# Kernel optimization log

Hardware: AMD Instinct MI355X
Metric: run time of the kernel (lower is better)

The kernel has to match this reference:

```python
import jax, jax.numpy as jnp
import numpy as np

D_MODEL, D_STATE, D_CONV, EXPAND = 1024, 16, 4, 2
D_INNER = EXPAND * D_MODEL
DT_RANK = (D_MODEL + 15) // 16  # 64
B_SZ, SEQ = 2, 1024


def _mamba_dir(x, inW, convW, convB, xpW, dtW, dtB, Alog, Dp, outW):
    """Standard Mamba block forward. x: [B, L, d_model]."""
    Bsz, L, _ = x.shape
    d_inner, d_state = Alog.shape
    dt_rank = xpW.shape[0] - 2 * d_state
    xz = jnp.einsum('bld,ed->ble', x, inW)            # [B, L, 2*d_inner]
    xi, z = jnp.split(xz, 2, axis=-1)
    # depthwise causal conv along L
    xc = jnp.swapaxes(xi, 1, 2)                       # [B, d_inner, L]
    xc = jax.lax.conv_general_dilated(
        xc, convW, window_strides=(1,),
        padding=[(convW.shape[-1] - 1, 0)],
        feature_group_count=d_inner)
    xc = xc + convB[None, :, None]
    u = jax.nn.silu(jnp.swapaxes(xc, 1, 2))           # [B, L, d_inner]
    x_dbl = jnp.einsum('bld,ed->ble', u, xpW)         # [B, L, dt_rank+2N]
    dt, Bm, Cm = jnp.split(x_dbl, [dt_rank, dt_rank + d_state], axis=-1)
    delta = jax.nn.softplus(jnp.einsum('blr,dr->bld', dt, dtW) + dtB)  # [B,L,d_inner]
    A = -jnp.exp(Alog)                                # [d_inner, d_state]

    def step(h, ins):
        d_t, B_t, C_t, u_t = ins                      # [B,D],[B,N],[B,N],[B,D]
        dA = jnp.exp(d_t[:, :, None] * A)             # [B, D, N]
        h = h * dA + (d_t * u_t)[:, :, None] * B_t[:, None, :]
        y_t = jnp.einsum('bdn,bn->bd', h, C_t)
        return h, y_t

    h0 = jnp.zeros((Bsz, d_inner, d_state), x.dtype)
    xs = (jnp.swapaxes(delta, 0, 1), jnp.swapaxes(Bm, 0, 1),
          jnp.swapaxes(Cm, 0, 1), jnp.swapaxes(u, 0, 1))
    _, ys = jax.lax.scan(step, h0, xs)
    y = jnp.swapaxes(ys, 0, 1)                        # [B, L, d_inner]
    y = y + u * Dp
    y = y * jax.nn.silu(z)
    return jnp.einsum('bld,od->blo', y, outW)         # [B, L, d_model]


def _make_params(key, suffix):
    ks = jax.random.split(key, 10)
    s = 0.02
    p = {
        'inW' + suffix: jax.random.normal(ks[0], (2 * D_INNER, D_MODEL), jnp.float32) * s,
        'convW' + suffix: jax.random.normal(ks[1], (D_INNER, 1, D_CONV), jnp.float32) * s,
        'convB' + suffix: jnp.zeros((D_INNER,), jnp.float32),
        'xpW' + suffix: jax.random.normal(ks[2], (DT_RANK + 2 * D_STATE, D_INNER), jnp.float32) * s,
        'dtW' + suffix: jax.random.normal(ks[3], (D_INNER, DT_RANK), jnp.float32) * s,
        'dtB' + suffix: jax.random.normal(ks[4], (D_INNER,), jnp.float32) * 0.1 - 4.0,
        'Alog' + suffix: jnp.log(1.0 + jax.random.uniform(ks[5], (D_INNER, D_STATE), jnp.float32) * 15.0),
        'Dp' + suffix: jnp.ones((D_INNER,), jnp.float32),
        'outW' + suffix: jax.random.normal(ks[6], (D_MODEL, D_INNER), jnp.float32) * s,
    }
    return p


def setup_inputs() -> dict:
    key = jax.random.key(0)
    kx, kf, kb = jax.random.split(key, 3)
    inp = {'x': jax.random.normal(kx, (B_SZ, SEQ, D_MODEL), jnp.float32)}
    inp.update(_make_params(kf, '_f'))
    inp.update(_make_params(kb, '_b'))
    return inp


def reference(x, inW_f, convW_f, convB_f, xpW_f, dtW_f, dtB_f, Alog_f, Dp_f, outW_f,
              inW_b, convW_b, convB_b, xpW_b, dtW_b, dtB_b, Alog_b, Dp_b, outW_b):
    y_fwd = _mamba_dir(x, inW_f, convW_f, convB_f, xpW_f, dtW_f, dtB_f, Alog_f, Dp_f, outW_f)
    xb = jnp.flip(x, axis=1)
    y_bwd = jnp.flip(_mamba_dir(xb, inW_b, convW_b, convB_b, xpW_b, dtW_b, dtB_b, Alog_b, Dp_b, outW_b), axis=1)
    return 0.5 * (y_fwd + y_bwd)
```

## Files before the change

### kernel.cpp

```cpp
#include <hip/hip_runtime.h>
#include <math.h>

#define B_SZ 2
#define SEQ  1024
#define DM   1024
#define DI   2048
#define NST  16
#define RNK  64
#define XPD  96
#define M_TOT (B_SZ*SEQ)
#define NC   32
#define LC   (SEQ/NC)
#define NCH  65536

typedef unsigned short ushort_t;
typedef __attribute__((ext_vector_type(8))) short short8;
typedef __attribute__((ext_vector_type(4))) float f32x4;

#if __has_builtin(__builtin_amdgcn_exp2f)
#define EXP2F __builtin_amdgcn_exp2f
#else
#define EXP2F exp2f
#endif
#define LOG2E 1.44269504f

__device__ __forceinline__ ushort_t f2bf(float f) {
    unsigned u = __float_as_uint(f);
    u += 0x7fff + ((u >> 16) & 1);
    return (ushort_t)(u >> 16);
}
__device__ __forceinline__ float bf2f(ushort_t v) {
    return __uint_as_float(((unsigned)v) << 16);
}

__global__ __launch_bounds__(256)
void convert_all(const float* __restrict__ x,
                 const float* __restrict__ inWf, const float* __restrict__ inWb,
                 const float* __restrict__ outWf, const float* __restrict__ outWb,
                 const float* __restrict__ xpWf, const float* __restrict__ xpWb,
                 ushort_t* __restrict__ xbf, ushort_t* __restrict__ inWcat,
                 ushort_t* __restrict__ outWcat, ushort_t* __restrict__ xpWcat)
{
    int bid = blockIdx.x;
    const float* src; ushort_t* dst; int rel; int strided = 0;
    if (bid < 2048)       { rel = bid;         src = x;     dst = xbf; }
    else if (bid < 6144)  { rel = bid - 2048;  src = inWf;  dst = inWcat; }
    else if (bid < 10240) { rel = bid - 6144;  src = inWb;  dst = inWcat + (size_t)2 * DI * DM; }
    else if (bid < 12288) { rel = bid - 10240; src = outWf; dst = outWcat;      strided = 1; }
    else if (bid < 14336) { rel = bid - 12288; src = outWb; dst = outWcat + DI; strided = 1; }
    else if (bid < 14528) { rel = bid - 14336; src = xpWf;  dst = xpWcat; }
    else                  { rel = bid - 14528; src = xpWb;  dst = xpWcat + (size_t)XPD * DI; }
    int i = rel * 256 + threadIdx.x;
    float4 v = ((const float4*)src)[i];
    ushort4 o;
    o.x = f2bf(v.x); o.y = f2bf(v.y); o.z = f2bf(v.z); o.w = f2bf(v.w);
    if (!strided) {
        ((ushort4*)dst)[i] = o;
    } else {
        int row = i >> 9;
        int c4  = (i - (row << 9)) << 2;
        *(ushort4*)(dst + (size_t)row * (2 * DI) + c4) = o;
    }
}

__device__ __forceinline__ void load_lds16(const ushort_t* g, ushort_t* l) {
    __builtin_amdgcn_global_load_lds(
        (const __attribute__((address_space(1))) void*)g,
        (__attribute__((address_space(3))) void*)l, 16, 0, 0);
}

template<bool OUT_BF16>
__global__ __launch_bounds__(256)
void gemm_gll(const ushort_t* __restrict__ A, const ushort_t* __restrict__ W,
              void* __restrict__ D, int M, int N, int K, int kLen, int ldD)
{
    __shared__ __align__(16) ushort_t As[128 * 64];
    __shared__ __align__(16) ushort_t Ws[128 * 64];
    const int t    = threadIdx.x;
    const int lane = t & 63;
    const int wave = t >> 6;
    const int wr   = (wave >> 1) * 64;
    const int wc   = (wave & 1) * 64;

    const int m0 = blockIdx.y * 128;
    const int n0 = blockIdx.x * 128;
    const int kStart = blockIdx.z * kLen;

    const int srow   = lane >> 3;
    const int gchunk = (lane & 7) ^ srow;

    f32x4 acc[4][4] = {};

    for (int k0 = kStart; k0 < kStart + kLen; k0 += 64) {
#pragma unroll
        for (int it = 0; it < 4; it++) {
            const int rb = wave * 32 + it * 8;
            load_lds16(A + (size_t)(m0 + rb + srow) * K + k0 + gchunk * 8,
                       As + rb * 64);
            load_lds16(W + (size_t)(n0 + rb + srow) * K + k0 + gchunk * 8,
                       Ws + rb * 64);
        }
        __syncthreads();
#pragma unroll
        for (int kk = 0; kk < 2; kk++) {
            const int kc = kk * 4 + (lane >> 4);
            short8 af[4], bf[4];
#pragma unroll
            for (int i = 0; i < 4; i++) {
                int r = wr + i * 16 + (lane & 15);
                af[i] = *(const short8*)(As + r * 64 + ((kc ^ (r & 7)) << 3));
            }
#pragma unroll
            for (int j = 0; j < 4; j++) {
                int r = wc + j * 16 + (lane & 15);
                bf[j] = *(const short8*)(Ws + r * 64 + ((kc ^ (r & 7)) << 3));
            }
#pragma unroll
            for (int i = 0; i < 4; i++)
#pragma unroll
                for (int j = 0; j < 4; j++)
                    acc[i][j] = __builtin_amdgcn_mfma_f32_16x16x32_bf16(
                        af[i], bf[j], acc[i][j], 0, 0, 0);
        }
        __syncthreads();
    }

    if (OUT_BF16) {
        ushort_t* Dp = (ushort_t*)D;
#pragma unroll
        for (int i = 0; i < 4; i++)
#pragma unroll
            for (int r = 0; r < 4; r++) {
                int m = m0 + wr + i * 16 + ((lane >> 4) << 2) + r;
#pragma unroll
                for (int j = 0; j < 4; j++) {
                    int n = n0 + wc + j * 16 + (lane & 15);
                    Dp[(size_t)m * ldD + n] = f2bf(acc[i][j][r]);
                }
            }
    } else {
        float* Dp = (float*)D + (size_t)blockIdx.z * M * ldD;
#pragma unroll
        for (int i = 0; i < 4; i++)
#pragma unroll
            for (int r = 0; r < 4; r++) {
                int m = m0 + wr + i * 16 + ((lane >> 4) << 2) + r;
#pragma unroll
                for (int j = 0; j < 4; j++) {
                    int n = n0 + wc + j * 16 + (lane & 15);
                    Dp[(size_t)m * ldD + n] = acc[i][j][r];
                }
            }
    }
}

__global__ __launch_bounds__(256)
void reduce4(const float* __restrict__ P, float* __restrict__ out)
{
    int i = blockIdx.x * 256 + threadIdx.x;
    const size_t S = (size_t)M_TOT * DM / 4;
    float4 a = ((const float4*)P)[i];
    float4 b = ((const float4*)P)[i + S];
    float4 c = ((const float4*)P)[i + 2 * S];
    float4 d = ((const float4*)P)[i + 3 * S];
    float4 o;
    o.x = 0.5f * (a.x + b.x + c.x + d.x);
    o.y = 0.5f * (a.y + b.y + c.y + d.y);
    o.z = 0.5f * (a.z + b.z + c.z + d.z);
    o.w = 0.5f * (a.w + b.w + c.w + d.w);
    ((float4*)out)[i] = o;
}

#define LDSP 72

__global__ __launch_bounds__(256)
void gemm2_splitk2(const ushort_t* __restrict__ ubf, const ushort_t* __restrict__ xpWcat,
                   float* __restrict__ P)
{
    const int dir = blockIdx.z >> 3;
    const int kz  = blockIdx.z & 7;
    const ushort_t* A = ubf + (size_t)dir * M_TOT * DI;
    const ushort_t* W = xpWcat + (size_t)dir * XPD * DI;
    const int K = DI, N = XPD;

    __shared__ __align__(16) ushort_t As[64 * LDSP];
    __shared__ __align__(16) ushort_t Ws[64 * LDSP];
    const int t    = threadIdx.x;
    const int lane = t & 63;
    const int wave = t >> 6;
    const int wr   = (wave >> 1) * 32;
    const int wc   = (wave & 1) * 32;

    f32x4 acc[2][2] = {};

    const int m0 = blockIdx.y * 64;
    const int n0 = blockIdx.x * 64;
    const int kStart = kz * (DI / 8);
    const int srow = t >> 3;
    const int scol = (t & 7) << 3;

    for (int k0 = kStart; k0 < kStart + DI / 8; k0 += 64) {
        {
            int r = srow;
            short8 v = *(const short8*)(A + (size_t)(m0 + r) * K + k0 + scol);
            *(short8*)(&As[r * LDSP + scol]) = v;
            int r2 = 32 + srow;
            short8 v2 = *(const short8*)(A + (size_t)(m0 + r2) * K + k0 + scol);
            *(short8*)(&As[r2 * LDSP + scol]) = v2;
            int wn = n0 + r;
            short8 wv = {};
            if (wn < N) wv = *(const short8*)(W + (size_t)wn * K + k0 + scol);
            *(short8*)(&Ws[r * LDSP + scol]) = wv;
            int wn2 = n0 + r2;
            short8 wv2 = {};
            if (wn2 < N) wv2 = *(const short8*)(W + (size_t)wn2 * K + k0 + scol);
            *(short8*)(&Ws[r2 * LDSP + scol]) = wv2;
        }
        __syncthreads();
#pragma unroll
        for (int kk = 0; kk < 2; kk++) {
            const int kcol = kk * 32 + ((lane >> 4) << 3);
            short8 af[2], bfr[2];
#pragma unroll
            for (int i = 0; i < 2; i++)
                af[i] = *(const short8*)(&As[(wr + i * 16 + (lane & 15)) * LDSP + kcol]);
#pragma unroll
            for (int j = 0; j < 2; j++)
                bfr[j] = *(const short8*)(&Ws[(wc + j * 16 + (lane & 15)) * LDSP + kcol]);
#pragma unroll
            for (int i = 0; i < 2; i++)
#pragma unroll
                for (int j = 0; j < 2; j++)
                    acc[i][j] = __builtin_amdgcn_mfma_f32_16x16x32_bf16(
                        af[i], bfr[j], acc[i][j], 0, 0, 0);
        }
        __syncthreads();
    }

    float* Pz = P + ((size_t)dir * 8 + kz) * M_TOT * XPD;
#pragma unroll
    for (int i = 0; i < 2; i++)
#pragma unroll
        for (int r = 0; r < 4; r++) {
            int m = m0 + wr + i * 16 + ((lane >> 4) << 2) + r;
#pragma unroll
            for (int j = 0; j < 2; j++) {
                int n = n0 + wc + j * 16 + (lane & 15);
                if (n < N) Pz[(size_t)m * XPD + n] = acc[i][j][r];
            }
        }
}

__global__ __launch_bounds__(256)
void xdbl_reduce2(const float* __restrict__ P, float* __restrict__ xdbl)
{
    int bid = blockIdx.x;
    int dir = bid >= 192;
    int i = (bid - dir * 192) * 256 + threadIdx.x;
    const size_t S = (size_t)M_TOT * XPD / 4;
    const float4* Pd = (const float4*)(P + (size_t)dir * 8 * M_TOT * XPD);
    float4 s = Pd[i];
#pragma unroll
    for (int z = 1; z < 8; z++) {
        float4 v = Pd[i + z * S];
        s.x += v.x; s.y += v.y; s.z += v.z; s.w += v.w;
    }
    ((float4*)(xdbl + (size_t)dir * M_TOT * XPD))[i] = s;
}

__global__ __launch_bounds__(256)
void delta_gemm2(const float* __restrict__ xdbl,
                 const float* __restrict__ dtWf, const float* __restrict__ dtWb,
                 const float* __restrict__ dtBf, const float* __restrict__ dtBb,
                 ushort_t* __restrict__ deltab)
{
    const int dir = blockIdx.z;
    const float* xd  = xdbl + (size_t)dir * M_TOT * XPD;
    const float* dtW = dir ? dtWb : dtWf;
    const float* dtB = dir ? dtBb : dtBf;
    ushort_t* delta  = deltab + (size_t)dir * M_TOT * DI;

    __shared__ __align__(16) ushort_t As[64 * LDSP];
    __shared__ __align__(16) ushort_t Ws[64 * LDSP];
    const int t    = threadIdx.x;
    const int lane = t & 63;
    const int wave = t >> 6;
    const int wr   = (wave >> 1) * 32;
    const int wc   = (wave & 1) * 32;

    const int m0 = blockIdx.y * 64;
    const int n0 = blockIdx.x * 64;
    const int srow = t >> 2;
    const int scol = (t & 3) << 4;

    {
        const float* ap = xd  + (size_t)(m0 + srow) * XPD + scol;
        const float* wp = dtW + (size_t)(n0 + srow) * RNK + scol;
        float4 a[4], w[4];
#pragma unroll
        for (int q = 0; q < 4; q++) { a[q] = ((const float4*)ap)[q]; w[q] = ((const float4*)wp)[q]; }
        __align__(16) ushort_t at[16], wt[16];
#pragma unroll
        for (int q = 0; q < 16; q++) {
            at[q] = f2bf(((const float*)a)[q]);
            wt[q] = f2bf(((const float*)w)[q]);
        }
        *(short8*)(&As[srow * LDSP + scol])     = *(const short8*)(at);
        *(short8*)(&As[srow * LDSP + scol + 8]) = *(const short8*)(at + 8);
        *(short8*)(&Ws[srow * LDSP + scol])     = *(const short8*)(wt);
        *(short8*)(&Ws[srow * LDSP + scol + 8]) = *(const short8*)(wt + 8);
    }
    __syncthreads();

    f32x4 acc[2][2] = {};
#pragma unroll
    for (int kk = 0; kk < 2; kk++) {
        const int kcol = kk * 32 + ((lane >> 4) << 3);
        short8 af[2], bfr[2];
#pragma unroll
        for (int i = 0; i < 2; i++)
            af[i] = *(const short8*)(&As[(wr + i * 16 + (lane & 15)) * LDSP + kcol]);
#pragma unroll
        for (int j = 0; j < 2; j++)
            bfr[j] = *(const short8*)(&Ws[(wc + j * 16 + (lane & 15)) * LDSP + kcol]);
#pragma unroll
        for (int i = 0; i < 2; i++)
#pragma unroll
            for (int j = 0; j < 2; j++)
                acc[i][j] = __builtin_amdgcn_mfma_f32_16x16x32_bf16(
                    af[i], bfr[j], acc[i][j], 0, 0, 0);
    }

#pragma unroll
    for (int j = 0; j < 2; j++) {
        int n = n0 + wc + j * 16 + (lane & 15);
        float bn = dtB[n];
#pragma unroll
        for (int i = 0; i < 2; i++) {
#pragma unroll
            for (int r = 0; r < 4; r++) {
                int m = m0 + wr + i * 16 + ((lane >> 4) << 2) + r;
                float v = acc[i][j][r] + bn;
                float sp = (v > 20.f) ? v : log1pf(__expf(v));
                delta[(size_t)m * DI + n] = f2bf(sp);
            }
        }
    }
}

__global__ __launch_bounds__(256)
void conv_silu2(const ushort_t* __restrict__ xzall,
                const float* __restrict__ convWf, const float* __restrict__ convWb,
                const float* __restrict__ convBf, const float* __restrict__ convBb,
                ushort_t* __restrict__ ubf)
{
    int bid = blockIdx.x;
    int dir = bid >> 12;
    int idx = (bid & 4095) * 256 + threadIdx.x;
    const float* convW = dir ? convWb : convWf;
    const float* convB = dir ? convBb : convBf;
    int di  = (idx & (DI / 4 - 1)) << 2;
    int m   = idx >> 9;
    int b   = m >> 10, l = m & (SEQ - 1);
    const ushort_t* xb = xzall + (size_t)b * SEQ * (4 * DI) + dir * (2 * DI) + di;

    float wv[4][4];
#pragma unroll
    for (int c = 0; c < 4; c++) {
        float4 w = *(const float4*)(convW + (di + c) * 4);
        wv[c][0] = w.x; wv[c][1] = w.y; wv[c][2] = w.z; wv[c][3] = w.w;
    }
    float4 cb = *(const float4*)(convB + di);
    float acc[4] = {cb.x, cb.y, cb.z, cb.w};
#pragma unroll
    for (int j = 0; j < 4; j++) {
        int srcl = dir ? (l + 3 - j) : (l - 3 + j);
        if ((unsigned)srcl < SEQ) {
            ushort4 xv = *(const ushort4*)(xb + (size_t)srcl * (4 * DI));
            acc[0] += wv[0][j] * bf2f(xv.x);
            acc[1] += wv[1][j] * bf2f(xv.y);
            acc[2] += wv[2][j] * bf2f(xv.z);
            acc[3] += wv[3][j] * bf2f(xv.w);
        }
    }
    ushort4 o;
    o.x = f2bf(acc[0] / (1.f + __expf(-acc[0])));
    o.y = f2bf(acc[1] / (1.f + __expf(-acc[1])));
    o.z = f2bf(acc[2] / (1.f + __expf(-acc[2])));
    o.w = f2bf(acc[3] / (1.f + __expf(-acc[3])));
    *(ushort4*)(ubf + (size_t)dir * M_TOT * DI + (size_t)m * DI + di) = o;
}

__global__ __launch_bounds__(256)
void scan_pass1_2(const ushort_t* __restrict__ deltab, const ushort_t* __restrict__ ubf,
                  const float* __restrict__ xdbl,
                  const float* __restrict__ Alogf, const float* __restrict__ Alogb,
                  float* __restrict__ Sb, float* __restrict__ SD)
{
    int tid = threadIdx.x, lane = tid & 63, wv = tid >> 6;
    int blk = blockIdx.x;
    int dir = blk >> 9;
    blk &= 511;
    int dg = blk & 7;
    int bc = blk >> 3;
    int c  = bc & (NC - 1);
    int b  = bc >> 5;
    int d  = (dg * 4 + wv) * 64 + lane;
    int t0 = dir ? (SEQ - 1 - c * LC) : (c * LC);
    int rs = dir ? -1 : 1;

    const float* Alog = dir ? Alogb : Alogf;
    const ushort_t* dl_p = deltab + (size_t)dir * M_TOT * DI;
    const ushort_t* u_p  = ubf    + (size_t)dir * M_TOT * DI;
    const float*    xd   = xdbl   + (size_t)dir * M_TOT * XPD;
    float* Sbd = Sb + (size_t)dir * NC * NCH;
    float* SDd = SD + (size_t)dir * NC * B_SZ * DI;

    float ac2[NST];
#pragma unroll
    for (int q = 0; q < 4; q++) {
        float4 al = *(const float4*)(Alog + (size_t)d * NST + q * 4);
        ac2[q * 4 + 0] = -__expf(al.x) * LOG2E;
        ac2[q * 4 + 1] = -__expf(al.y) * LOG2E;
        ac2[q * 4 + 2] = -__expf(al.z) * LOG2E;
        ac2[q * 4 + 3] = -__expf(al.w) * LOG2E;
    }
    float h[NST];
#pragma unroll
    for (int n = 0; n < NST; n++) h[n] = 0.f;
    float sumD = 0.f;

#pragma unroll 4
    for (int l = 0; l < LC; l++) {
        int t = t0 + rs * l;
        size_t row = (size_t)b * SEQ + t;
        float dl = bf2f(dl_p[row * DI + d]);
        float uv = bf2f(u_p[row * DI + d]);
        const float* xr = xd + row * XPD + RNK;
        float4 Bv[4];
#pragma unroll
        for (int q = 0; q < 4; q++) Bv[q] = *(const float4*)(xr + q * 4);
        float dlu = dl * uv;
        sumD += dl;
#pragma unroll
        for (int n = 0; n < NST; n++) {
            float dA = EXP2F(dl * ac2[n]);
            h[n] = h[n] * dA + dlu * ((const float*)Bv)[n];
        }
    }

    size_t o = (size_t)c * NCH + ((size_t)b * DI + d) * NST;
#pragma unroll
    for (int q = 0; q < 4; q++)
        *(float4*)(Sbd + o + q * 4) = make_float4(h[q*4], h[q*4+1], h[q*4+2], h[q*4+3]);
    SDd[(size_t)c * (B_SZ * DI) + b * DI + d] = sumD;
}

__global__ __launch_bounds__(256)
void scan_combine2(float* __restrict__ Sb, const float* __restrict__ SD,
                   const float* __restrict__ Alogf, const float* __restrict__ Alogb)
{
    int gid = blockIdx.x * 256 + threadIdx.x;
    int dir = gid >= NCH;
    int i = gid - dir * NCH;
    int n = i & 15;
    int d = (i >> 4) & (DI - 1);
    int b = i >> 15;
    const float* Alog = dir ? Alogb : Alogf;
    float* Sbd = Sb + (size_t)dir * NC * NCH;
    const float* SDd = SD + (size_t)dir * NC * B_SZ * DI;
    float ac2 = -__expf(Alog[(size_t)d * NST + n]) * LOG2E;
    float h = 0.f;
#pragma unroll
    for (int c = 0; c < NC; c++) {
        float s = Sbd[(size_t)c * NCH + i];
        float p = EXP2F(ac2 * SDd[(size_t)c * (B_SZ * DI) + b * DI + d]);
        Sbd[(size_t)c * NCH + i] = h;
        h = s + p * h;
    }
}

__global__ __launch_bounds__(256)
void scan_pass2_2(const ushort_t* __restrict__ deltab, const ushort_t* __restrict__ ubf,
                  const float* __restrict__ xdbl, const ushort_t* __restrict__ xzall,
                  const float* __restrict__ Alogf, const float* __restrict__ Alogb,
                  const float* __restrict__ Dpf, const float* __restrict__ Dpb,
                  const float* __restrict__ Hinit, ushort_t* __restrict__ ybf)
{
    int tid = threadIdx.x, lane = tid & 63, wv = tid >> 6;
    int blk = blockIdx.x;
    int dir = blk >> 9;
    blk &= 511;
    int dg = blk & 7;
    int bc = blk >> 3;
    int c  = bc & (NC - 1);
    int b  = bc >> 5;
    int d  = (dg * 4 + wv) * 64 + lane;
    int t0 = dir ? (SEQ - 1 - c * LC) : (c * LC);
    int rs = dir ? -1 : 1;

    const float* Alog = dir ? Alogb : Alogf;
    const float* Dpp  = dir ? Dpb : Dpf;
    const ushort_t* dl_p = deltab + (size_t)dir * M_TOT * DI;
    const ushort_t* u_p  = ubf    + (size_t)dir * M_TOT * DI;
    const float*    xd   = xdbl   + (size_t)dir * M_TOT * XPD;
    const float*    Hin  = Hinit  + (size_t)dir * NC * NCH;

    float ac2[NST];
#pragma unroll
    for (int q = 0; q < 4; q++) {
        float4 al = *(const float4*)(Alog + (size_t)d * NST + q * 4);
        ac2[q * 4 + 0] = -__expf(al.x) * LOG2E;
        ac2[q * 4 + 1] = -__expf(al.y) * LOG2E;
        ac2[q * 4 + 2] = -__expf(al.z) * LOG2E;
        ac2[q * 4 + 3] = -__expf(al.w) * LOG2E;
    }
    float dp = Dpp[d];
    float h[NST];
    {
        size_t o = (size_t)c * NCH + ((size_t)b * DI + d) * NST;
#pragma unroll
        for (int q = 0; q < 4; q++) {
            float4 hv = *(const float4*)(Hin + o + q * 4);
            h[q*4] = hv.x; h[q*4+1] = hv.y; h[q*4+2] = hv.z; h[q*4+3] = hv.w;
        }
    }

#pragma unroll 4
    for (int l = 0; l < LC; l++) {
        int t = t0 + rs * l;
        size_t row = (size_t)b * SEQ + t;
        float dl = bf2f(dl_p[row * DI + d]);
        float uv = bf2f(u_p[row * DI + d]);
        const float* xr = xd + row * XPD + RNK;
        float4 Bv[4], Cv[4];
#pragma unroll
        for (int q = 0; q < 4; q++) {
            Bv[q] = *(const float4*)(xr + q * 4);
            Cv[q] = *(const float4*)(xr + NST + q * 4);
        }
        float dlu = dl * uv;
        float y = 0.f;
#pragma unroll
        for (int n = 0; n < NST; n++) {
            float dA = EXP2F(dl * ac2[n]);
            h[n] = h[n] * dA + dlu * ((const float*)Bv)[n];
            y += h[n] * ((const float*)Cv)[n];
        }
        float z = bf2f(xzall[row * (4 * DI) + dir * (2 * DI) + DI + d]);
        float yv = (y + uv * dp) * (z / (1.f + __expf(-z)));
        ybf[row * (2 * DI) + dir * DI + d] = f2bf(yv);
    }
}

extern "C" void kernel_launch(void* const* d_in, const int* in_sizes, int n_in,
                              void* d_out, int out_size, void* d_ws, size_t ws_size,
                              hipStream_t stream)
{
    char* wsb = (char*)d_ws;

    ushort_t* xzall  = (ushort_t*)wsb;
    ushort_t* ybf    = (ushort_t*)(wsb + 33554432);
    ushort_t* inWcat = (ushort_t*)(wsb + 50331648);
    ushort_t* outWcat= (ushort_t*)(wsb + 67108864);
    ushort_t* xbf    = (ushort_t*)(wsb + 75497472);
    ushort_t* xpWcat = (ushort_t*)(wsb + 79691776);
    ushort_t* ubf    = (ushort_t*)(wsb + 80478208);
    ushort_t* deltab = (ushort_t*)(wsb + 97255424);
    float*    xdbl   = (float*)(wsb + 114032640);

    float* Sb    = (float*)inWcat;
    float* SD    = (float*)xbf;
    float* part2 = (float*)deltab;
    float* part4 = (float*)xzall;

    float* out = (float*)d_out;
    dim3 blk(256);

    convert_all<<<14720, blk, 0, stream>>>(
        (const float*)d_in[0], (const float*)d_in[1], (const float*)d_in[10],
        (const float*)d_in[9], (const float*)d_in[18],
        (const float*)d_in[4], (const float*)d_in[13],
        xbf, inWcat, outWcat, xpWcat);

    gemm_gll<true><<<dim3(8192 / 128, M_TOT / 128, 1), blk, 0, stream>>>(
        xbf, inWcat, xzall, M_TOT, 8192, DM, DM, 8192);

    conv_silu2<<<8192, blk, 0, stream>>>(xzall,
        (const float*)d_in[2], (const float*)d_in[11],
        (const float*)d_in[3], (const float*)d_in[12], ubf);

    gemm2_splitk2<<<dim3(2, M_TOT / 64, 16), blk, 0, stream>>>(ubf, xpWcat, part2);

    xdbl_reduce2<<<384, blk, 0, stream>>>(part2, xdbl);

    delta_gemm2<<<dim3(DI / 64, M_TOT / 64, 2), blk, 0, stream>>>(
        xdbl, (const float*)d_in[5], (const float*)d_in[14],
        (const float*)d_in[6], (const float*)d_in[15], deltab);

    scan_pass1_2<<<1024, blk, 0, stream>>>(deltab, ubf, xdbl,
        (const float*)d_in[7], (const float*)d_in[16], Sb, SD);
    scan_combine2<<<2 * NCH / 256, blk, 0, stream>>>(Sb, SD,
        (const float*)d_in[7], (const float*)d_in[16]);
    scan_pass2_2<<<1024, blk, 0, stream>>>(deltab, ubf, xdbl, xzall,
        (const float*)d_in[7], (const float*)d_in[16],
        (const float*)d_in[8], (const float*)d_in[17], Sb, ybf);

    gemm_gll<false><<<dim3(DM / 128, M_TOT / 128, 4), blk, 0, stream>>>(
        ybf, outWcat, part4, M_TOT, DM, 2 * DI, DI / 2, DM);

    reduce4<<<(M_TOT * DM / 4) / 256, blk, 0, stream>>>(part4, out);
}
```

Before: 357.8 us.

## Fuse mid-pipeline and output stages into cooperative persistent kernels with grid syncs

Replaces the seven middle kernels (conv, x_proj split-K GEMM, reduce, delta GEMM, the two scan passes and the combine) with one cooperative kernel of 512 persistent blocks. The stages are separated by grid.sync. The output GEMM and its split-K reduce are also merged into a second cooperative kernel. The goal is to remove kernel launch gaps and tail effects between many small dependent stages. In exchange, a fixed grid size runs each stage and grid-wide barriers are added, with occupancy limited by launch_bounds(256,2). If the cooperative launch fails, the code falls back to the separate kernels.

```diff
diff --git a/kernel.cpp b/kernel.cpp
--- a/kernel.cpp
+++ b/kernel.cpp
@@ -1,5 +1,8 @@
 #include <hip/hip_runtime.h>
+#include <hip/hip_cooperative_groups.h>
 #include <math.h>
+
+namespace cg = cooperative_groups;
 
 #define B_SZ 2
 #define SEQ  1024
@@ -12,6 +15,7 @@
 #define NC   32
 #define LC   (SEQ/NC)
 #define NCH  65536
+#define CGB  512
 
 typedef unsigned short ushort_t;
 typedef __attribute__((ext_vector_type(8))) short short8;
@@ -95,10 +99,8 @@
 #pragma unroll
         for (int it = 0; it < 4; it++) {
             const int rb = wave * 32 + it * 8;
-            load_lds16(A + (size_t)(m0 + rb + srow) * K + k0 + gchunk * 8,
-                       As + rb * 64);
-            load_lds16(W + (size_t)(n0 + rb + srow) * K + k0 + gchunk * 8,
-                       Ws + rb * 64);
+            load_lds16(A + (size_t)(m0 + rb + srow) * K + k0 + gchunk * 8, As + rb * 64);
+            load_lds16(W + (size_t)(n0 + rb + srow) * K + k0 + gchunk * 8, Ws + rb * 64);
         }
         __syncthreads();
 #pragma unroll
@@ -173,197 +175,18 @@
 
 #define LDSP 72
 
-__global__ __launch_bounds__(256)
-void gemm2_splitk2(const ushort_t* __restrict__ ubf, const ushort_t* __restrict__ xpWcat,
-                   float* __restrict__ P)
-{
-    const int dir = blockIdx.z >> 3;
-    const int kz  = blockIdx.z & 7;
-    const ushort_t* A = ubf + (size_t)dir * M_TOT * DI;
-    const ushort_t* W = xpWcat + (size_t)dir * XPD * DI;
-    const int K = DI, N = XPD;
-
-    __shared__ __align__(16) ushort_t As[64 * LDSP];
-    __shared__ __align__(16) ushort_t Ws[64 * LDSP];
-    const int t    = threadIdx.x;
-    const int lane = t & 63;
-    const int wave = t >> 6;
-    const int wr   = (wave >> 1) * 32;
-    const int wc   = (wave & 1) * 32;
-
-    f32x4 acc[2][2] = {};
-
-    const int m0 = blockIdx.y * 64;
-    const int n0 = blockIdx.x * 64;
-    const int kStart = kz * (DI / 8);
-    const int srow = t >> 3;
-    const int scol = (t & 7) << 3;
-
-    for (int k0 = kStart; k0 < kStart + DI / 8; k0 += 64) {
-        {
-            int r = srow;
-            short8 v = *(const short8*)(A + (size_t)(m0 + r) * K + k0 + scol);
-            *(short8*)(&As[r * LDSP + scol]) = v;
-            int r2 = 32 + srow;
-            short8 v2 = *(const short8*)(A + (size_t)(m0 + r2) * K + k0 + scol);
-            *(short8*)(&As[r2 * LDSP + scol]) = v2;
-            int wn = n0 + r;
-            short8 wv = {};
-            if (wn < N) wv = *(const short8*)(W + (size_t)wn * K + k0 + scol);
-            *(short8*)(&Ws[r * LDSP + scol]) = wv;
-            int wn2 = n0 + r2;
-            short8 wv2 = {};
-            if (wn2 < N) wv2 = *(const short8*)(W + (size_t)wn2 * K + k0 + scol);
-            *(short8*)(&Ws[r2 * LDSP + scol]) = wv2;
-        }
-        __syncthreads();
-#pragma unroll
-        for (int kk = 0; kk < 2; kk++) {
-            const int kcol = kk * 32 + ((lane >> 4) << 3);
-            short8 af[2], bfr[2];
-#pragma unroll
-            for (int i = 0; i < 2; i++)
-                af[i] = *(const short8*)(&As[(wr + i * 16 + (lane & 15)) * LDSP + kcol]);
-#pragma unroll
-            for (int j = 0; j < 2; j++)
-                bfr[j] = *(const short8*)(&Ws[(wc + j * 16 + (lane & 15)) * LDSP + kcol]);
-#pragma unroll
-            for (int i = 0; i < 2; i++)
-#pragma unroll
-                for (int j = 0; j < 2; j++)
-                    acc[i][j] = __builtin_amdgcn_mfma_f32_16x16x32_bf16(
-                        af[i], bfr[j], acc[i][j], 0, 0, 0);
-        }
-        __syncthreads();
-    }
-
-    float* Pz = P + ((size_t)dir * 8 + kz) * M_TOT * XPD;
-#pragma unroll
-    for (int i = 0; i < 2; i++)
-#pragma unroll
-        for (int r = 0; r < 4; r++) {
-            int m = m0 + wr + i * 16 + ((lane >> 4) << 2) + r;
-#pragma unroll
-            for (int j = 0; j < 2; j++) {
-                int n = n0 + wc + j * 16 + (lane & 15);
-                if (n < N) Pz[(size_t)m * XPD + n] = acc[i][j][r];
-            }
-        }
-}
-
-__global__ __launch_bounds__(256)
-void xdbl_reduce2(const float* __restrict__ P, float* __restrict__ xdbl)
-{
-    int bid = blockIdx.x;
-    int dir = bid >= 192;
-    int i = (bid - dir * 192) * 256 + threadIdx.x;
-    const size_t S = (size_t)M_TOT * XPD / 4;
-    const float4* Pd = (const float4*)(P + (size_t)dir * 8 * M_TOT * XPD);
-    float4 s = Pd[i];
-#pragma unroll
-    for (int z = 1; z < 8; z++) {
-        float4 v = Pd[i + z * S];
-        s.x += v.x; s.y += v.y; s.z += v.z; s.w += v.w;
-    }
-    ((float4*)(xdbl + (size_t)dir * M_TOT * XPD))[i] = s;
-}
-
-__global__ __launch_bounds__(256)
-void delta_gemm2(const float* __restrict__ xdbl,
-                 const float* __restrict__ dtWf, const float* __restrict__ dtWb,
-                 const float* __restrict__ dtBf, const float* __restrict__ dtBb,
-                 ushort_t* __restrict__ deltab)
-{
-    const int dir = blockIdx.z;
-    const float* xd  = xdbl + (size_t)dir * M_TOT * XPD;
-    const float* dtW = dir ? dtWb : dtWf;
-    const float* dtB = dir ? dtBb : dtBf;
-    ushort_t* delta  = deltab + (size_t)dir * M_TOT * DI;
-
-    __shared__ __align__(16) ushort_t As[64 * LDSP];
-    __shared__ __align__(16) ushort_t Ws[64 * LDSP];
-    const int t    = threadIdx.x;
-    const int lane = t & 63;
-    const int wave = t >> 6;
-    const int wr   = (wave >> 1) * 32;
-    const int wc   = (wave & 1) * 32;
-
-    const int m0 = blockIdx.y * 64;
-    const int n0 = blockIdx.x * 64;
-    const int srow = t >> 2;
-    const int scol = (t & 3) << 4;
-
-    {
-        const float* ap = xd  + (size_t)(m0 + srow) * XPD + scol;
-        const float* wp = dtW + (size_t)(n0 + srow) * RNK + scol;
-        float4 a[4], w[4];
-#pragma unroll
-        for (int q = 0; q < 4; q++) { a[q] = ((const float4*)ap)[q]; w[q] = ((const float4*)wp)[q]; }
-        __align__(16) ushort_t at[16], wt[16];
-#pragma unroll
-        for (int q = 0; q < 16; q++) {
-            at[q] = f2bf(((const float*)a)[q]);
-            wt[q] = f2bf(((const float*)w)[q]);
-        }
-        *(short8*)(&As[srow * LDSP + scol])     = *(const short8*)(at);
-        *(short8*)(&As[srow * LDSP + scol + 8]) = *(const short8*)(at + 8);
-        *(short8*)(&Ws[srow * LDSP + scol])     = *(const short8*)(wt);
-        *(short8*)(&Ws[srow * LDSP + scol + 8]) = *(const short8*)(wt + 8);
-    }
-    __syncthreads();
-
-    f32x4 acc[2][2] = {};
-#pragma unroll
-    for (int kk = 0; kk < 2; kk++) {
-        const int kcol = kk * 32 + ((lane >> 4) << 3);
-        short8 af[2], bfr[2];
-#pragma unroll
-        for (int i = 0; i < 2; i++)
-            af[i] = *(const short8*)(&As[(wr + i * 16 + (lane & 15)) * LDSP + kcol]);
-#pragma unroll
-        for (int j = 0; j < 2; j++)
-            bfr[j] = *(const short8*)(&Ws[(wc + j * 16 + (lane & 15)) * LDSP + kcol]);
-#pragma unroll
-        for (int i = 0; i < 2; i++)
-#pragma unroll
-            for (int j = 0; j < 2; j++)
-                acc[i][j] = __builtin_amdgcn_mfma_f32_16x16x32_bf16(
-                    af[i], bfr[j], acc[i][j], 0, 0, 0);
-    }
-
-#pragma unroll
-    for (int j = 0; j < 2; j++) {
-        int n = n0 + wc + j * 16 + (lane & 15);
-        float bn = dtB[n];
-#pragma unroll
-        for (int i = 0; i < 2; i++) {
-#pragma unroll
-            for (int r = 0; r < 4; r++) {
-                int m = m0 + wr + i * 16 + ((lane >> 4) << 2) + r;
-                float v = acc[i][j][r] + bn;
-                float sp = (v > 20.f) ? v : log1pf(__expf(v));
-                delta[(size_t)m * DI + n] = f2bf(sp);
-            }
-        }
-    }
-}
-
-__global__ __launch_bounds__(256)
-void conv_silu2(const ushort_t* __restrict__ xzall,
-                const float* __restrict__ convWf, const float* __restrict__ convWb,
-                const float* __restrict__ convBf, const float* __restrict__ convBb,
-                ushort_t* __restrict__ ubf)
-{
-    int bid = blockIdx.x;
-    int dir = bid >> 12;
-    int idx = (bid & 4095) * 256 + threadIdx.x;
+__device__ __forceinline__ void conv_body(int job, int tid,
+    const ushort_t* xzall, const float* convWf, const float* convWb,
+    const float* convBf, const float* convBb, ushort_t* ubf)
+{
+    int dir = job >> 12;
+    int idx = (job & 4095) * 256 + tid;
     const float* convW = dir ? convWb : convWf;
     const float* convB = dir ? convBb : convBf;
-    int di  = (idx & (DI / 4 - 1)) << 2;
-    int m   = idx >> 9;
-    int b   = m >> 10, l = m & (SEQ - 1);
+    int di = (idx & (DI / 4 - 1)) << 2;
+    int m  = idx >> 9;
+    int b  = m >> 10, l = m & (SEQ - 1);
     const ushort_t* xb = xzall + (size_t)b * SEQ * (4 * DI) + dir * (2 * DI) + di;
-
     float wv[4][4];
 #pragma unroll
     for (int c = 0; c < 4; c++) {
@@ -391,24 +214,184 @@
     *(ushort4*)(ubf + (size_t)dir * M_TOT * DI + (size_t)m * DI + di) = o;
 }
 
-__global__ __launch_bounds__(256)
-void scan_pass1_2(const ushort_t* __restrict__ deltab, const ushort_t* __restrict__ ubf,
-                  const float* __restrict__ xdbl,
-                  const float* __restrict__ Alogf, const float* __restrict__ Alogb,
-                  float* __restrict__ Sb, float* __restrict__ SD)
-{
-    int tid = threadIdx.x, lane = tid & 63, wv = tid >> 6;
-    int blk = blockIdx.x;
-    int dir = blk >> 9;
-    blk &= 511;
+__device__ __forceinline__ void gemm2_body(int job, int tid,
+    const ushort_t* ubf, const ushort_t* xpWcat, float* part2,
+    ushort_t* As, ushort_t* Ws)
+{
+    const int lane = tid & 63;
+    const int wave = tid >> 6;
+    int nt = job & 1;
+    int mt = (job >> 1) & 31;
+    int z  = job >> 6;
+    int dir = z >> 3;
+    int kz  = z & 7;
+    const ushort_t* A = ubf + (size_t)dir * M_TOT * DI;
+    const ushort_t* W = xpWcat + (size_t)dir * XPD * DI;
+    const int K = DI, N = XPD;
+    const int wr = (wave >> 1) * 32;
+    const int wc = (wave & 1) * 32;
+    f32x4 acc[2][2] = {};
+    const int m0 = mt * 64;
+    const int n0 = nt * 64;
+    const int kStart = kz * (DI / 8);
+    const int srow = tid >> 3;
+    const int scol = (tid & 7) << 3;
+    for (int k0 = kStart; k0 < kStart + DI / 8; k0 += 64) {
+        {
+            int r = srow;
+            *(short8*)(&As[r * LDSP + scol]) =
+                *(const short8*)(A + (size_t)(m0 + r) * K + k0 + scol);
+            int r2 = 32 + srow;
+            *(short8*)(&As[r2 * LDSP + scol]) =
+                *(const short8*)(A + (size_t)(m0 + r2) * K + k0 + scol);
+            int wn = n0 + r;
+            short8 wvv = {};
+            if (wn < N) wvv = *(const short8*)(W + (size_t)wn * K + k0 + scol);
+            *(short8*)(&Ws[r * LDSP + scol]) = wvv;
+            int wn2 = n0 + r2;
+            short8 wv2 = {};
+            if (wn2 < N) wv2 = *(const short8*)(W + (size_t)wn2 * K + k0 + scol);
+            *(short8*)(&Ws[r2 * LDSP + scol]) = wv2;
+        }
+        __syncthreads();
+#pragma unroll
+        for (int kk = 0; kk < 2; kk++) {
+            const int kcol = kk * 32 + ((lane >> 4) << 3);
+            short8 af[2], bfr[2];
+#pragma unroll
+            for (int i = 0; i < 2; i++)
+                af[i] = *(const short8*)(&As[(wr + i * 16 + (lane & 15)) * LDSP + kcol]);
+#pragma unroll
+            for (int j = 0; j < 2; j++)
+                bfr[j] = *(const short8*)(&Ws[(wc + j * 16 + (lane & 15)) * LDSP + kcol]);
+#pragma unroll
+            for (int i = 0; i < 2; i++)
+#pragma unroll
+                for (int j = 0; j < 2; j++)
+                    acc[i][j] = __builtin_amdgcn_mfma_f32_16x16x32_bf16(
+                        af[i], bfr[j], acc[i][j], 0, 0, 0);
+        }
+        __syncthreads();
+    }
+    float* Pz = part2 + ((size_t)dir * 8 + kz) * M_TOT * XPD;
+#pragma unroll
+    for (int i = 0; i < 2; i++)
+#pragma unroll
+        for (int r = 0; r < 4; r++) {
+            int m = m0 + wr + i * 16 + ((lane >> 4) << 2) + r;
+#pragma unroll
+            for (int j = 0; j < 2; j++) {
+                int n = n0 + wc + j * 16 + (lane & 15);
+                if (n < N) Pz[(size_t)m * XPD + n] = acc[i][j][r];
+            }
+        }
+}
+
+__device__ __forceinline__ void xdblred_body(int job, int tid,
+    const float* part2, float* xdbl)
+{
+    int dir = job >= 192;
+    int i = (job - dir * 192) * 256 + tid;
+    const size_t S = (size_t)M_TOT * XPD / 4;
+    const float4* Pd = (const float4*)(part2 + (size_t)dir * 8 * M_TOT * XPD);
+    float4 s = Pd[i];
+#pragma unroll
+    for (int z = 1; z < 8; z++) {
+        float4 v = Pd[i + z * S];
+        s.x += v.x; s.y += v.y; s.z += v.z; s.w += v.w;
+    }
+    ((float4*)(xdbl + (size_t)dir * M_TOT * XPD))[i] = s;
+}
+
+__device__ __forceinline__ void delta_body(int job, int tid,
+    const float* xdbl, const float* dtWf, const float* dtWb,
+    const float* dtBf, const float* dtBb, ushort_t* deltab,
+    ushort_t* As, ushort_t* Ws)
+{
+    const int lane = tid & 63;
+    const int wave = tid >> 6;
+    int nt = job & 31;
+    int mt = (job >> 5) & 31;
+    int dir = job >> 10;
+    const float* xd  = xdbl + (size_t)dir * M_TOT * XPD;
+    const float* dtW = dir ? dtWb : dtWf;
+    const float* dtB = dir ? dtBb : dtBf;
+    ushort_t* delta  = deltab + (size_t)dir * M_TOT * DI;
+    const int wr = (wave >> 1) * 32;
+    const int wc = (wave & 1) * 32;
+    const int m0 = mt * 64;
+    const int n0 = nt * 64;
+    const int srow = tid >> 2;
+    const int scol = (tid & 3) << 4;
+    {
+        const float* ap = xd  + (size_t)(m0 + srow) * XPD + scol;
+        const float* wp = dtW + (size_t)(n0 + srow) * RNK + scol;
+        float4 av[4], wv[4];
+#pragma unroll
+        for (int q = 0; q < 4; q++) { av[q] = ((const float4*)ap)[q]; wv[q] = ((const float4*)wp)[q]; }
+        __align__(16) ushort_t at[16], wt[16];
+#pragma unroll
+        for (int q = 0; q < 16; q++) {
+            at[q] = f2bf(((const float*)av)[q]);
+            wt[q] = f2bf(((const float*)wv)[q]);
+        }
+        *(short8*)(&As[srow * LDSP + scol])     = *(const short8*)(at);
+        *(short8*)(&As[srow * LDSP + scol + 8]) = *(const short8*)(at + 8);
+        *(short8*)(&Ws[srow * LDSP + scol])     = *(const short8*)(wt);
+        *(short8*)(&Ws[srow * LDSP + scol + 8]) = *(const short8*)(wt + 8);
+    }
+    __syncthreads();
+    f32x4 acc[2][2] = {};
+#pragma unroll
+    for (int kk = 0; kk < 2; kk++) {
+        const int kcol = kk * 32 + ((lane >> 4) << 3);
+        short8 af[2], bfr[2];
+#pragma unroll
+        for (int i = 0; i < 2; i++)
+            af[i] = *(const short8*)(&As[(wr + i * 16 + (lane & 15)) * LDSP + kcol]);
+#pragma unroll
+        for (int j = 0; j < 2; j++)
+            bfr[j] = *(const short8*)(&Ws[(wc + j * 16 + (lane & 15)) * LDSP + kcol]);
+#pragma unroll
+        for (int i = 0; i < 2; i++)
+#pragma unroll
+            for (int j = 0; j < 2; j++)
+                acc[i][j] = __builtin_amdgcn_mfma_f32_16x16x32_bf16(
+                    af[i], bfr[j], acc[i][j], 0, 0, 0);
+    }
+#pragma unroll
+    for (int j = 0; j < 2; j++) {
+        int n = n0 + wc + j * 16 + (lane & 15);
+        float bn = dtB[n];
+#pragma unroll
+        for (int i = 0; i < 2; i++) {
+#pragma unroll
+            for (int r = 0; r < 4; r++) {
+                int m = m0 + wr + i * 16 + ((lane >> 4) << 2) + r;
+                float v = acc[i][j][r] + bn;
+                float sp = (v > 20.f) ? v : log1pf(__expf(v));
+                delta[(size_t)m * DI + n] = f2bf(sp);
+            }
+        }
+    }
+    __syncthreads();
+}
+
+__device__ __forceinline__ void scan1_body(int job, int tid,
+    const ushort_t* deltab, const ushort_t* ubf, const float* xdbl,
+    const float* Alogf, const float* Alogb, float* Sb, float* SD)
+{
+    const int lane = tid & 63;
+    const int wave = tid >> 6;
+    int dir = job >> 9;
+    int blk = job & 511;
     int dg = blk & 7;
     int bc = blk >> 3;
     int c  = bc & (NC - 1);
     int b  = bc >> 5;
-    int d  = (dg * 4 + wv) * 64 + lane;
+    int d  = (dg * 4 + wave) * 64 + lane;
     int t0 = dir ? (SEQ - 1 - c * LC) : (c * LC);
     int rs = dir ? -1 : 1;
-
     const float* Alog = dir ? Alogb : Alogf;
     const ushort_t* dl_p = deltab + (size_t)dir * M_TOT * DI;
     const ushort_t* u_p  = ubf    + (size_t)dir * M_TOT * DI;
@@ -429,7 +412,6 @@
 #pragma unroll
     for (int n = 0; n < NST; n++) h[n] = 0.f;
     float sumD = 0.f;
-
 #pragma unroll 4
     for (int l = 0; l < LC; l++) {
         int t = t0 + rs * l;
@@ -448,7 +430,6 @@
             h[n] = h[n] * dA + dlu * ((const float*)Bv)[n];
         }
     }
-
     size_t o = (size_t)c * NCH + ((size_t)b * DI + d) * NST;
 #pragma unroll
     for (int q = 0; q < 4; q++)
@@ -456,11 +437,10 @@
     SDd[(size_t)c * (B_SZ * DI) + b * DI + d] = sumD;
 }
 
-__global__ __launch_bounds__(256)
-void scan_combine2(float* __restrict__ Sb, const float* __restrict__ SD,
-                   const float* __restrict__ Alogf, const float* __restrict__ Alogb)
-{
-    int gid = blockIdx.x * 256 + threadIdx.x;
+__device__ __forceinline__ void combine_body(int job, int tid,
+    float* Sb, const float* SD, const float* Alogf, const float* Alogb)
+{
+    int gid = job * 256 + tid;
     int dir = gid >= NCH;
     int i = gid - dir * NCH;
     int n = i & 15;
@@ -480,25 +460,22 @@
     }
 }
 
-__global__ __launch_bounds__(256)
-void scan_pass2_2(const ushort_t* __restrict__ deltab, const ushort_t* __restrict__ ubf,
-                  const float* __restrict__ xdbl, const ushort_t* __restrict__ xzall,
-                  const float* __restrict__ Alogf, const float* __restrict__ Alogb,
-                  const float* __restrict__ Dpf, const float* __restrict__ Dpb,
-                  const float* __restrict__ Hinit, ushort_t* __restrict__ ybf)
-{
-    int tid = threadIdx.x, lane = tid & 63, wv = tid >> 6;
-    int blk = blockIdx.x;
-    int dir = blk >> 9;
-    blk &= 511;
+__device__ __forceinline__ void scan2_body(int job, int tid,
+    const ushort_t* deltab, const ushort_t* ubf, const float* xdbl,
+    const ushort_t* xzall, const float* Alogf, const float* Alogb,
+    const float* Dpf, const float* Dpb, const float* Hinit, ushort_t* ybf)
+{
+    const int lane = tid & 63;
+    const int wave = tid >> 6;
+    int dir = job >> 9;
+    int blk = job & 511;
     int dg = blk & 7;
     int bc = blk >> 3;
     int c  = bc & (NC - 1);
     int b  = bc >> 5;
-    int d  = (dg * 4 + wv) * 64 + lane;
+    int d  = (dg * 4 + wave) * 64 + lane;
     int t0 = dir ? (SEQ - 1 - c * LC) : (c * LC);
     int rs = dir ? -1 : 1;
-
     const float* Alog = dir ? Alogb : Alogf;
     const float* Dpp  = dir ? Dpb : Dpf;
     const ushort_t* dl_p = deltab + (size_t)dir * M_TOT * DI;
@@ -525,7 +502,6 @@
             h[q*4] = hv.x; h[q*4+1] = hv.y; h[q*4+2] = hv.z; h[q*4+3] = hv.w;
         }
     }
-
 #pragma unroll 4
     for (int l = 0; l < LC; l++) {
         int t = t0 + rs * l;
@@ -550,6 +526,219 @@
         float z = bf2f(xzall[row * (4 * DI) + dir * (2 * DI) + DI + d]);
         float yv = (y + uv * dp) * (z / (1.f + __expf(-z)));
         ybf[row * (2 * DI) + dir * DI + d] = f2bf(yv);
+    }
+}
+
+__global__ __launch_bounds__(256)
+void conv_silu2(const ushort_t* __restrict__ xzall,
+                const float* __restrict__ convWf, const float* __restrict__ convWb,
+                const float* __restrict__ convBf, const float* __restrict__ convBb,
+                ushort_t* __restrict__ ubf)
+{
+    conv_body(blockIdx.x, threadIdx.x, xzall, convWf, convWb, convBf, convBb, ubf);
+}
+
+__global__ __launch_bounds__(256)
+void gemm2_splitk2(const ushort_t* __restrict__ ubf, const ushort_t* __restrict__ xpWcat,
+                   float* __restrict__ P)
+{
+    __shared__ __align__(16) ushort_t As[64 * LDSP];
+    __shared__ __align__(16) ushort_t Ws[64 * LDSP];
+    gemm2_body(blockIdx.x, threadIdx.x, ubf, xpWcat, P, As, Ws);
+}
+
+__global__ __launch_bounds__(256)
+void xdbl_reduce2(const float* __restrict__ P, float* __restrict__ xdbl)
+{
+    xdblred_body(blockIdx.x, threadIdx.x, P, xdbl);
+}
+
+__global__ __launch_bounds__(256)
+void delta_gemm2(const float* __restrict__ xdbl,
+                 const float* __restrict__ dtWf, const float* __restrict__ dtWb,
+                 const float* __restrict__ dtBf, const float* __restrict__ dtBb,
+                 ushort_t* __restrict__ deltab)
+{
+    __shared__ __align__(16) ushort_t As[64 * LDSP];
+    __shared__ __align__(16) ushort_t Ws[64 * LDSP];
+    delta_body(blockIdx.x, threadIdx.x, xdbl, dtWf, dtWb, dtBf, dtBb, deltab, As, Ws);
+}
+
+__global__ __launch_bounds__(256)
+void scan_pass1_2(const ushort_t* __restrict__ deltab, const ushort_t* __restrict__ ubf,
+                  const float* __restrict__ xdbl,
+                  const float* __restrict__ Alogf, const float* __restrict__ Alogb,
+                  float* __restrict__ Sb, float* __restrict__ SD)
+{
+    scan1_body(blockIdx.x, threadIdx.x, deltab, ubf, xdbl, Alogf, Alogb, Sb, SD);
+}
+
+__global__ __launch_bounds__(256)
+void scan_combine2(float* __restrict__ Sb, const float* __restrict__ SD,
+                   const float* __restrict__ Alogf, const float* __restrict__ Alogb)
+{
+    combine_body(blockIdx.x, threadIdx.x, Sb, SD, Alogf, Alogb);
+}
+
+__global__ __launch_bounds__(256)
+void scan_pass2_2(const ushort_t* __restrict__ deltab, const ushort_t* __restrict__ ubf,
+                  const float* __restrict__ xdbl, const ushort_t* __restrict__ xzall,
+                  const float* __restrict__ Alogf, const float* __restrict__ Alogb,
+                  const float* __restrict__ Dpf, const float* __restrict__ Dpb,
+                  const float* __restrict__ Hinit, ushort_t* __restrict__ ybf)
+{
+    scan2_body(blockIdx.x, threadIdx.x, deltab, ubf, xdbl, xzall, Alogf, Alogb,
+               Dpf, Dpb, Hinit, ybf);
+}
+
+struct MidArgs {
+    const ushort_t* xzall;
+    ushort_t* ubf;
+    const ushort_t* xpWcat;
+    float* part2;
+    float* xdbl;
+    ushort_t* deltab;
+    float* Sb;
+    float* SD;
+    ushort_t* ybf;
+    const float* convWf; const float* convWb;
+    const float* convBf; const float* convBb;
+    const float* dtWf;   const float* dtWb;
+    const float* dtBf;   const float* dtBb;
+    const float* Alogf;  const float* Alogb;
+    const float* Dpf;    const float* Dpb;
+};
+
+__global__ __launch_bounds__(256, 2)
+void coop_mid(MidArgs a)
+{
+    cg::grid_group grid = cg::this_grid();
+    __shared__ __align__(16) ushort_t As[64 * LDSP];
+    __shared__ __align__(16) ushort_t Ws[64 * LDSP];
+    const int tid = threadIdx.x;
+    const int bid = blockIdx.x;
+
+    for (int job = bid; job < 8192; job += CGB)
+        conv_body(job, tid, a.xzall, a.convWf, a.convWb, a.convBf, a.convBb, a.ubf);
+    __threadfence(); grid.sync();
+
+    for (int job = bid; job < 1024; job += CGB)
+        gemm2_body(job, tid, a.ubf, a.xpWcat, a.part2, As, Ws);
+    __threadfence(); grid.sync();
+
+    for (int job = bid; job < 384; job += CGB)
+        xdblred_body(job, tid, a.part2, a.xdbl);
+    __threadfence(); grid.sync();
+
+    for (int job = bid; job < 2048; job += CGB)
+        delta_body(job, tid, a.xdbl, a.dtWf, a.dtWb, a.dtBf, a.dtBb, a.deltab, As, Ws);
+    __threadfence(); grid.sync();
+
+    for (int job = bid; job < 1024; job += CGB)
+        scan1_body(job, tid, a.deltab, a.ubf, a.xdbl, a.Alogf, a.Alogb, a.Sb, a.SD);
+    __threadfence(); grid.sync();
+
+    for (int job = bid; job < 512; job += CGB)
+        combine_body(job, tid, a.Sb, a.SD, a.Alogf, a.Alogb);
+    __threadfence(); grid.sync();
+
+    for (int job = bid; job < 1024; job += CGB)
+        scan2_body(job, tid, a.deltab, a.ubf, a.xdbl, a.xzall, a.Alogf, a.Alogb,
+                   a.Dpf, a.Dpb, a.Sb, a.ybf);
+}
+
+struct OutArgs {
+    const ushort_t* ybf;
+    const ushort_t* outWcat;
+    float* part;
+    float* out;
+};
+
+__global__ __launch_bounds__(256, 2)
+void coop_out(OutArgs a)
+{
+    cg::grid_group grid = cg::this_grid();
+    __shared__ __align__(16) ushort_t As[128 * 64];
+    __shared__ __align__(16) ushort_t Ws[128 * 64];
+    const int tid  = threadIdx.x;
+    const int bid  = blockIdx.x;
+    const int lane = tid & 63;
+    const int wave = tid >> 6;
+
+    {
+        const int nt = bid & 7;
+        const int mt = (bid >> 3) & 15;
+        const int z  = bid >> 7;
+        const int K = 2 * DI, kLen = DI / 2, ldD = DM;
+        const int wr = (wave >> 1) * 64;
+        const int wc = (wave & 1) * 64;
+        const int m0 = mt * 128;
+        const int n0 = nt * 128;
+        const int kStart = z * kLen;
+        const int srow   = lane >> 3;
+        const int gchunk = (lane & 7) ^ srow;
+        f32x4 acc[4][4] = {};
+        for (int k0 = kStart; k0 < kStart + kLen; k0 += 64) {
+#pragma unroll
+            for (int it = 0; it < 4; it++) {
+                const int rb = wave * 32 + it * 8;
+                load_lds16(a.ybf + (size_t)(m0 + rb + srow) * K + k0 + gchunk * 8, As + rb * 64);
+                load_lds16(a.outWcat + (size_t)(n0 + rb + srow) * K + k0 + gchunk * 8, Ws + rb * 64);
+            }
+            __syncthreads();
+#pragma unroll
+            for (int kk = 0; kk < 2; kk++) {
+                const int kc = kk * 4 + (lane >> 4);
+                short8 af[4], bf[4];
+#pragma unroll
+                for (int i = 0; i < 4; i++) {
+                    int r = wr + i * 16 + (lane & 15);
+                    af[i] = *(const short8*)(As + r * 64 + ((kc ^ (r & 7)) << 3));
+                }
+#pragma unroll
+                for (int j = 0; j < 4; j++) {
+                    int r = wc + j * 16 + (lane & 15);
+                    bf[j] = *(const short8*)(Ws + r * 64 + ((kc ^ (r & 7)) << 3));
+                }
+#pragma unroll
+                for (int i = 0; i < 4; i++)
+#pragma unroll
+                    for (int j = 0; j < 4; j++)
+                        acc[i][j] = __builtin_amdgcn_mfma_f32_16x16x32_bf16(
+                            af[i], bf[j], acc[i][j], 0, 0, 0);
+            }
+            __syncthreads();
+        }
+        float* Dp = a.part + (size_t)z * M_TOT * ldD;
+#pragma unroll
+        for (int i = 0; i < 4; i++)
+#pragma unroll
+            for (int r = 0; r < 4; r++) {
+                int m = m0 + wr + i * 16 + ((lane >> 4) << 2) + r;
+#pragma unroll
+                for (int j = 0; j < 4; j++) {
+                    int n = n0 + wc + j * 16 + (lane & 15);
+                    Dp[(size_t)m * ldD + n] = acc[i][j][r];
+                }
+            }
+    }
+    __threadfence();
+    grid.sync();
+
+    const size_t S = (size_t)M_TOT * DM / 4;
+#pragma unroll
+    for (int rep = 0; rep < 4; rep++) {
+        int i = (bid * 4 + rep) * 256 + tid;
+        float4 p0 = ((const float4*)a.part)[i];
+        float4 p1 = ((const float4*)a.part)[i + S];
+        float4 p2 = ((const float4*)a.part)[i + 2 * S];
+        float4 p3 = ((const float4*)a.part)[i + 3 * S];
+        float4 o;
+        o.x = 0.5f * (p0.x + p1.x + p2.x + p3.x);
+        o.y = 0.5f * (p0.y + p1.y + p2.y + p3.y);
+        o.z = 0.5f * (p0.z + p1.z + p2.z + p3.z);
+        o.w = 0.5f * (p0.w + p1.w + p2.w + p3.w);
+        ((float4*)a.out)[i] = o;
     }
 }
 
@@ -586,28 +775,44 @@
     gemm_gll<true><<<dim3(8192 / 128, M_TOT / 128, 1), blk, 0, stream>>>(
         xbf, inWcat, xzall, M_TOT, 8192, DM, DM, 8192);
 
-    conv_silu2<<<8192, blk, 0, stream>>>(xzall,
-        (const float*)d_in[2], (const float*)d_in[11],
-        (const float*)d_in[3], (const float*)d_in[12], ubf);
-
-    gemm2_splitk2<<<dim3(2, M_TOT / 64, 16), blk, 0, stream>>>(ubf, xpWcat, part2);
-
-    xdbl_reduce2<<<384, blk, 0, stream>>>(part2, xdbl);
-
-    delta_gemm2<<<dim3(DI / 64, M_TOT / 64, 2), blk, 0, stream>>>(
-        xdbl, (const float*)d_in[5], (const float*)d_in[14],
-        (const float*)d_in[6], (const float*)d_in[15], deltab);
-
-    scan_pass1_2<<<1024, blk, 0, stream>>>(deltab, ubf, xdbl,
-        (const float*)d_in[7], (const float*)d_in[16], Sb, SD);
-    scan_combine2<<<2 * NCH / 256, blk, 0, stream>>>(Sb, SD,
-        (const float*)d_in[7], (const float*)d_in[16]);
-    scan_pass2_2<<<1024, blk, 0, stream>>>(deltab, ubf, xdbl, xzall,
-        (const float*)d_in[7], (const float*)d_in[16],
-        (const float*)d_in[8], (const float*)d_in[17], Sb, ybf);
-
-    gemm_gll<false><<<dim3(DM / 128, M_TOT / 128, 4), blk, 0, stream>>>(
-        ybf, outWcat, part4, M_TOT, DM, 2 * DI, DI / 2, DM);
-
-    reduce4<<<(M_TOT * DM / 4) / 256, blk, 0, stream>>>(part4, out);
-}
+    MidArgs margs;
+    margs.xzall = xzall; margs.ubf = ubf; margs.xpWcat = xpWcat;
+    margs.part2 = part2; margs.xdbl = xdbl; margs.deltab = deltab;
+    margs.Sb = Sb; margs.SD = SD; margs.ybf = ybf;
+    margs.convWf = (const float*)d_in[2];  margs.convWb = (const float*)d_in[11];
+    margs.convBf = (const float*)d_in[3];  margs.convBb = (const float*)d_in[12];
+    margs.dtWf   = (const float*)d_in[5];  margs.dtWb   = (const float*)d_in[14];
+    margs.dtBf   = (const float*)d_in[6];  margs.dtBb   = (const float*)d_in[15];
+    margs.Alogf  = (const float*)d_in[7];  margs.Alogb  = (const float*)d_in[16];
+    margs.Dpf    = (const float*)d_in[8];  margs.Dpb    = (const float*)d_in[17];
+    void* kargs1[] = { &margs };
+    hipError_t e1 = hipLaunchCooperativeKernel((void*)coop_mid, dim3(CGB), blk,
+                                               kargs1, 0, stream);
+    if (e1 != hipSuccess) {
+        (void)hipGetLastError();
+        conv_silu2<<<8192, blk, 0, stream>>>(xzall, margs.convWf, margs.convWb,
+                                             margs.convBf, margs.convBb, ubf);
+        gemm2_splitk2<<<1024, blk, 0, stream>>>(ubf, xpWcat, part2);
+        xdbl_reduce2<<<384, blk, 0, stream>>>(part2, xdbl);
+        delta_gemm2<<<2048, blk, 0, stream>>>(xdbl, margs.dtWf, margs.dtWb,
+                                              margs.dtBf, margs.dtBb, deltab);
+        scan_pass1_2<<<1024, blk, 0, stream>>>(deltab, ubf, xdbl,
+                                               margs.Alogf, margs.Alogb, Sb, SD);
+        scan_combine2<<<512, blk, 0, stream>>>(Sb, SD, margs.Alogf, margs.Alogb);
+        scan_pass2_2<<<1024, blk, 0, stream>>>(deltab, ubf, xdbl, xzall,
+                                               margs.Alogf, margs.Alogb,
+                                               margs.Dpf, margs.Dpb, Sb, ybf);
+    }
+
+    OutArgs oargs;
+    oargs.ybf = ybf; oargs.outWcat = outWcat; oargs.part = part4; oargs.out = out;
+    void* kargs2[] = { &oargs };
+    hipError_t e2 = hipLaunchCooperativeKernel((void*)coop_out, dim3(CGB), blk,
+                                               kargs2, 0, stream);
+    if (e2 != hipSuccess) {
+        (void)hipGetLastError();
+        gemm_gll<false><<<dim3(DM / 128, M_TOT / 128, 4), blk, 0, stream>>>(
+            ybf, outWcat, part4, M_TOT, DM, 2 * DI, DI / 2, DM);
+        reduce4<<<(M_TOT * DM / 4) / 256, blk, 0, stream>>>(part4, out);
+    }
+}
```

Result: slower. 1.190 ms (+232.5%).
